# Kernel optimization log

Hardware: AMD Instinct MI355X
Metric: run time of the kernel (lower is better)

Reference implementation:

```python
import jax, jax.numpy as jnp
import numpy as np

N_NODES = 100000
N_EDGES = 100000
N_MAP = 128
EPS = 1e-5


def _gn1(x, g, b):
    # GroupNorm with 1 group == per-row normalization over channels, affine per channel
    m = jnp.mean(x, axis=-1, keepdims=True)
    v = jnp.mean((x - m) ** 2, axis=-1, keepdims=True)
    return (x - m) * jax.lax.rsqrt(v + EPS) * g + b


def setup_inputs() -> dict:
    key = jax.random.key(0)
    ks = jax.random.split(key, 16)
    s = 0.02
    d = N_MAP
    inp = {
        'nodes': jax.random.normal(ks[0], (N_NODES, 8), jnp.float32),
        'indexes': jax.random.randint(ks[1], (N_EDGES, 28), 0, N_NODES, jnp.int64)
            if jax.config.jax_enable_x64 else jax.random.randint(ks[1], (N_EDGES, 28), 0, N_NODES, jnp.int32),
        'mask': jnp.full((14,), N_EDGES, dtype=jnp.int32),
        'in1_W': jax.random.normal(ks[2], (d, 2), jnp.float32) * s,
        'in1_b': jnp.zeros((d,), jnp.float32),
        'in2_W': jax.random.normal(ks[3], (d, d), jnp.float32) * s,
        'in_g': jnp.ones((d,), jnp.float32),
        'in_bg': jnp.zeros((d,), jnp.float32),
        'seg1_W': jax.random.normal(ks[4], (d, 2), jnp.float32) * s,
        'seg1_b': jnp.zeros((d,), jnp.float32),
        'seg2_W': jax.random.normal(ks[5], (d, d), jnp.float32) * s,
        'seg_g': jnp.ones((d,), jnp.float32),
        'seg_bg': jnp.zeros((d,), jnp.float32),
        'meta_W': jax.random.normal(ks[6], (d, d + 4), jnp.float32) * s,
        'meta_g': jnp.ones((d,), jnp.float32),
        'meta_bg': jnp.zeros((d,), jnp.float32),
        'ctr_W': jax.random.normal(ks[7], (4, d, d), jnp.float32) * s,
        'edge_W': jax.random.normal(ks[8], (4, 14, d, d), jnp.float32) * s,
        'norm_g': jnp.ones((4, d), jnp.float32),
        'norm_bg': jnp.zeros((4, d), jnp.float32),
        'ctr2_W': jax.random.normal(ks[9], (4, d, d), jnp.float32) * s,
        'ctr2_g': jnp.ones((4, d), jnp.float32),
        'ctr2_bg': jnp.zeros((4, d), jnp.float32),
    }
    return inp


def reference(nodes, indexes, mask, in1_W, in1_b, in2_W, in_g, in_bg,
              seg1_W, seg1_b, seg2_W, seg_g, seg_bg, meta_W, meta_g, meta_bg,
              ctr_W, edge_W, norm_g, norm_bg, ctr2_W, ctr2_g, ctr2_bg):
    relu = jax.nn.relu
    # input / seg branches: Linear+ReLU then bias-free Linear + GroupNorm(1)
    feat = _gn1(relu(nodes[:, :2] @ in1_W.T + in1_b) @ in2_W.T, in_g, in_bg)
    feat = feat + _gn1(relu(nodes[:, 2:4] @ seg1_W.T + seg1_b) @ seg2_W.T, seg_g, seg_bg)
    feat = relu(feat)
    # meta: Linear(n_map+4 -> n_map, bias-free) + GN + ReLU
    feat = relu(_gn1(jnp.concatenate([feat, nodes[:, 4:]], axis=1) @ meta_W.T, meta_g, meta_bg))
    res = feat
    E = indexes.shape[0]
    eid = jnp.arange(E)
    for i in range(4):
        temp = feat @ ctr_W[i].T
        # 14 edge types in column order: pre0..pre5, right, suc0..suc5, left
        for t in range(14):
            valid = (eid < mask[t])[:, None]          # [E,1]
            src = jnp.where(valid[:, 0], indexes[:, 2 * t + 1], 0)
            dst = jnp.where(valid[:, 0], indexes[:, 2 * t], 0)
            msg = jnp.where(valid, feat[src] @ edge_W[i, t].T, 0.0)  # [E, d]
            temp = temp.at[dst].add(msg)
        feat = relu(_gn1(temp, norm_g[i], norm_bg[i]))
        feat = _gn1(feat @ ctr2_W[i].T, ctr2_g[i], ctr2_bg[i])
        feat = relu(feat + res)
        res = feat
    return (feat, nodes[:, :2])
```

## Files before the change

kernel.cpp:

```cpp
#include <hip/hip_runtime.h>
#include <hip/hip_bf16.h>

#define NN 100000
#define NE 100000
#define NCNT (14 * NN)
#define LP 136
#define LP2 168
#define SCAN_CHUNK 4096
#define NSCB ((NCNT + SCAN_CHUNK - 1) / SCAN_CHUNK)

typedef __bf16 bf16;
typedef __bf16 bf16x8 __attribute__((ext_vector_type(8)));
typedef float  f32x4  __attribute__((ext_vector_type(4)));


template<int PITCH, int COLS>
__device__ inline void stageWB(const bf16* __restrict__ Wg, bf16* Wl) {
    constexpr int NV = 128 * COLS / 8;
    for (int i = threadIdx.x; i < NV; i += 256) {
        const int e = i * 8;
        const int r = e / COLS, c = e % COLS;
        *(float4*)(&Wl[r * PITCH + c]) = ((const float4*)Wg)[i];
    }
}

__device__ inline void stageA(const bf16* __restrict__ A, bf16* Al, int row0) {
    const int r = threadIdx.x >> 2, q = threadIdx.x & 3;
    float4* d = (float4*)(&Al[r * LP + q * 32]);
    const int row = row0 + r;
    if (row < NN) {
        const float4* s = (const float4*)(A + (size_t)row * 128 + q * 32);
        float4 a0 = s[0], a1 = s[1], a2 = s[2], a3 = s[3];
        d[0] = a0; d[1] = a1; d[2] = a2; d[3] = a3;
    } else {
        float4 z = {0.f, 0.f, 0.f, 0.f};
        d[0] = z; d[1] = z; d[2] = z; d[3] = z;
    }
}

template<int PITCH, int KSTEPS>
__device__ inline void mmaT(const bf16* Al, const bf16* Wl, int m0, int lane, f32x4 acc[8]) {
#pragma unroll
    for (int kk = 0; kk < KSTEPS; ++kk) {
        bf16x8 a = *(const bf16x8*)(&Al[(m0 + (lane & 15)) * PITCH + kk * 32 + (lane >> 4) * 8]);
#pragma unroll
        for (int n = 0; n < 8; ++n) {
            bf16x8 b = *(const bf16x8*)(&Wl[(n * 16 + (lane & 15)) * PITCH + kk * 32 + (lane >> 4) * 8]);
            acc[n] = __builtin_amdgcn_mfma_f32_16x16x32_bf16(a, b, acc[n], 0, 0, 0);
        }
    }
}

__device__ inline void zacc(f32x4 acc[8]) {
    f32x4 z = {0.f, 0.f, 0.f, 0.f};
#pragma unroll
    for (int n = 0; n < 8; ++n) acc[n] = z;
}

__device__ inline void gnstats(const f32x4 acc[8], float mean[4], float rs[4]) {
    float s1[4], s2[4];
#pragma unroll
    for (int r = 0; r < 4; ++r) { s1[r] = 0.f; s2[r] = 0.f; }
#pragma unroll
    for (int n = 0; n < 8; ++n)
#pragma unroll
        for (int r = 0; r < 4; ++r) { float v = acc[n][r]; s1[r] += v; s2[r] += v * v; }
#pragma unroll
    for (int off = 1; off < 16; off <<= 1) {
#pragma unroll
        for (int r = 0; r < 4; ++r) {
            s1[r] += __shfl_xor(s1[r], off, 64);
            s2[r] += __shfl_xor(s2[r], off, 64);
        }
    }
#pragma unroll
    for (int r = 0; r < 4; ++r) {
        const float m = s1[r] * 0.0078125f;
        const float v = fmaxf(s2[r] * 0.0078125f - m * m, 0.f);
        mean[r] = m;
        rs[r] = rsqrtf(v + 1e-5f);
    }
}


__global__ void k_cvt(const float* __restrict__ s, bf16* __restrict__ d, int n) {
    for (int i = blockIdx.x * 256 + threadIdx.x; i < n; i += gridDim.x * 256)
        d[i] = (bf16)s[i];
}

__global__ void k_cvt_meta(const float* __restrict__ s, bf16* __restrict__ d) {
    for (int i = blockIdx.x * 256 + threadIdx.x; i < 128 * 160; i += gridDim.x * 256) {
        const int r = i / 160, c = i % 160;
        d[i] = (bf16)(c < 132 ? s[r * 132 + c] : 0.f);
    }
}


__global__ __launch_bounds__(256) void k_count(const int* __restrict__ idx,
                                               const int* __restrict__ mask,
                                               int* __restrict__ cnt) {
    __shared__ int lim[14];
    if (threadIdx.x < 14) lim[threadIdx.x] = min(mask[threadIdx.x], NE);
    __syncthreads();
    for (int i = blockIdx.x * 256 + threadIdx.x; i < 14 * NE; i += gridDim.x * 256) {
        const int e = i / 14, t = i - e * 14;
        if (e < lim[t]) atomicAdd(&cnt[t * NN + idx[(size_t)e * 28 + 2 * t]], 1);
    }
}

__global__ __launch_bounds__(256) void k_scanA(const int* __restrict__ cnt,
                                               int* __restrict__ ptr,
                                               int* __restrict__ tot) {
    __shared__ int sm[256];
    const int tid = threadIdx.x;
    const int base = blockIdx.x * SCAN_CHUNK + tid * 16;
    int v[16]; int run = 0;
#pragma unroll
    for (int j = 0; j < 16; ++j) {
        const int x = (base + j < NCNT) ? cnt[base + j] : 0;
        v[j] = run; run += x;
    }
    sm[tid] = run; __syncthreads();
    for (int d = 1; d < 256; d <<= 1) {
        int t = 0;
        if (tid >= d) t = sm[tid - d];
        __syncthreads();
        sm[tid] += t;
        __syncthreads();
    }
    const int off = sm[tid] - run;
#pragma unroll
    for (int j = 0; j < 16; ++j)
        if (base + j < NCNT) ptr[base + j] = v[j] + off;
    if (tid == 255) tot[blockIdx.x] = sm[255];
}

__global__ void k_scanB(int* __restrict__ tot) {
    if (threadIdx.x == 0 && blockIdx.x == 0) {
        int acc = 0;
        for (int b = 0; b < NSCB; ++b) { const int t = tot[b]; tot[b] = acc; acc += t; }
        tot[NSCB] = acc;
    }
}

__global__ __launch_bounds__(256) void k_scanC(int* __restrict__ ptr,
                                               int* __restrict__ cursor,
                                               const int* __restrict__ tot) {
    const int base = blockIdx.x * SCAN_CHUNK;
    const int o = tot[blockIdx.x];
    for (int j = threadIdx.x; j < SCAN_CHUNK; j += 256) {
        const int i = base + j;
        if (i < NCNT) { const int p = ptr[i] + o; ptr[i] = p; cursor[i] = p; }
    }
    if (blockIdx.x == 0 && threadIdx.x == 0) ptr[NCNT] = tot[NSCB];
}

__global__ __launch_bounds__(256) void k_fill(const int* __restrict__ idx,
                                              const int* __restrict__ mask,
                                              int* __restrict__ cursor,
                                              int* __restrict__ elist) {
    __shared__ int lim[14];
    if (threadIdx.x < 14) lim[threadIdx.x] = min(mask[threadIdx.x], NE);
    __syncthreads();
    for (int i = blockIdx.x * 256 + threadIdx.x; i < 14 * NE; i += gridDim.x * 256) {
        const int e = i / 14, t = i - e * 14;
        if (e < lim[t]) {
            const int dst = idx[(size_t)e * 28 + 2 * t];
            const int pos = atomicAdd(&cursor[t * NN + dst], 1);
            elist[pos] = e;
        }
    }
}

__global__ __launch_bounds__(256) void k_sortseg(const int* __restrict__ ptr,
                                                 int* __restrict__ elist,
                                                 const int* __restrict__ idx) {
    for (int i = blockIdx.x * 256 + threadIdx.x; i < NCNT; i += gridDim.x * 256) {
        const int s = ptr[i], e2 = ptr[i + 1];
        for (int a = s + 1; a < e2; ++a) {
            const int key = elist[a];
            int b = a - 1;
            while (b >= s && elist[b] > key) { elist[b + 1] = elist[b]; --b; }
            elist[b + 1] = key;
        }
        const int t = i / NN;
        for (int j = s; j < e2; ++j)
            elist[j] = idx[(size_t)elist[j] * 28 + 2 * t + 1];
    }
}


__global__ __launch_bounds__(256) void k_in(
    const float* __restrict__ nodes,
    const float* __restrict__ in1W, const float* __restrict__ in1b,
    const bf16* __restrict__ wIn2,
    const float* __restrict__ ing, const float* __restrict__ inbg,
    const float* __restrict__ seg1W, const float* __restrict__ seg1b,
    const bf16* __restrict__ wSeg2,
    const float* __restrict__ segg, const float* __restrict__ segbg,
    bf16* __restrict__ outPre)
{
    __shared__ __align__(16) bf16 Wl[128 * LP];
    __shared__ __align__(16) bf16 Al[64 * LP];
    __shared__ float w0[128], w1[128], bb[128];
    __shared__ float xs[64][4];
    const int tid = threadIdx.x;
    const int row0 = blockIdx.x * 64;
    if (tid < 64) {
        const int row = row0 + tid;
        float4 x = {0.f, 0.f, 0.f, 0.f};
        if (row < NN) x = *(const float4*)(nodes + (size_t)row * 8);
        xs[tid][0] = x.x; xs[tid][1] = x.y; xs[tid][2] = x.z; xs[tid][3] = x.w;
    }
    if (tid < 128) { w0[tid] = in1W[tid * 2]; w1[tid] = in1W[tid * 2 + 1]; bb[tid] = in1b[tid]; }
    stageWB<LP, 128>(wIn2, Wl);
    __syncthreads();
    for (int i = tid; i < 64 * 128; i += 256) {
        const int r = i >> 7, j = i & 127;
        Al[r * LP + j] = (bf16)fmaxf(xs[r][0] * w0[j] + xs[r][1] * w1[j] + bb[j], 0.f);
    }
    __syncthreads();
    const int lane = tid & 63, m0 = (tid >> 6) * 16;
    f32x4 accP[8]; zacc(accP);
    mmaT<LP, 4>(Al, Wl, m0, lane, accP);
    __syncthreads();
    if (tid < 128) { w0[tid] = seg1W[tid * 2]; w1[tid] = seg1W[tid * 2 + 1]; bb[tid] = seg1b[tid]; }
    stageWB<LP, 128>(wSeg2, Wl);
    __syncthreads();
    for (int i = tid; i < 64 * 128; i += 256) {
        const int r = i >> 7, j = i & 127;
        Al[r * LP + j] = (bf16)fmaxf(xs[r][2] * w0[j] + xs[r][3] * w1[j] + bb[j], 0.f);
    }
    __syncthreads();
    f32x4 accQ[8]; zacc(accQ);
    mmaT<LP, 4>(Al, Wl, m0, lane, accQ);

    float mP[4], rP[4], mQ[4], rQ[4];
    gnstats(accP, mP, rP);
    gnstats(accQ, mQ, rQ);
    float gP[8], bP[8], gQ[8], bQ[8];
#pragma unroll
    for (int n = 0; n < 8; ++n) {
        const int c = n * 16 + (lane & 15);
        gP[n] = ing[c]; bP[n] = inbg[c]; gQ[n] = segg[c]; bQ[n] = segbg[c];
    }
#pragma unroll
    for (int r = 0; r < 4; ++r) {
        const int row = row0 + m0 + (lane >> 4) * 4 + r;
        if (row < NN) {
#pragma unroll
            for (int n = 0; n < 8; ++n) {
                const float yp = (accP[n][r] - mP[r]) * rP[r] * gP[n] + bP[n];
                const float yq = (accQ[n][r] - mQ[r]) * rQ[r] * gQ[n] + bQ[n];
                outPre[(size_t)row * 128 + n * 16 + (lane & 15)] = (bf16)fmaxf(yp + yq, 0.f);
            }
        }
    }
}


__global__ __launch_bounds__(256) void k_meta(
    const bf16* __restrict__ Apre, const float* __restrict__ nodes,
    const bf16* __restrict__ Wg,
    const float* __restrict__ g, const float* __restrict__ bg,
    float* __restrict__ featF, bf16* __restrict__ featB)
{
    __shared__ __align__(16) bf16 Wl[128 * LP2];
    __shared__ __align__(16) bf16 Al[64 * LP2];
    const int row0 = blockIdx.x * 64;
    stageWB<LP2, 160>(Wg, Wl);
    {
        const int r = threadIdx.x >> 2, q = threadIdx.x & 3;
        float4* d = (float4*)(&Al[r * LP2 + q * 32]);
        const int row = row0 + r;
        if (row < NN) {
            const float4* s = (const float4*)(Apre + (size_t)row * 128 + q * 32);
            float4 a0 = s[0], a1 = s[1], a2 = s[2], a3 = s[3];
            d[0] = a0; d[1] = a1; d[2] = a2; d[3] = a3;
        } else {
            float4 z = {0.f, 0.f, 0.f, 0.f};
            d[0] = z; d[1] = z; d[2] = z; d[3] = z;
        }
    }
    if (threadIdx.x < 64) {
        const int rr = threadIdx.x, row = row0 + rr;
        bf16* d = &Al[rr * LP2 + 128];
        if (row < NN) {
            const float4 x = *(const float4*)(nodes + (size_t)row * 8 + 4);
            d[0] = (bf16)x.x; d[1] = (bf16)x.y; d[2] = (bf16)x.z; d[3] = (bf16)x.w;
        } else {
            d[0] = (bf16)0.f; d[1] = (bf16)0.f; d[2] = (bf16)0.f; d[3] = (bf16)0.f;
        }
#pragma unroll
        for (int c = 4; c < 32; ++c) d[c] = (bf16)0.f;
    }
    __syncthreads();
    const int lane = threadIdx.x & 63, m0 = (threadIdx.x >> 6) * 16;
    f32x4 acc[8]; zacc(acc);
    mmaT<LP2, 5>(Al, Wl, m0, lane, acc);

    float mean[4], rs[4];
    gnstats(acc, mean, rs);
    float gv[8], bv[8];
#pragma unroll
    for (int n = 0; n < 8; ++n) { const int c = n * 16 + (lane & 15); gv[n] = g[c]; bv[n] = bg[c]; }
#pragma unroll
    for (int r = 0; r < 4; ++r) {
        const int row = row0 + m0 + (lane >> 4) * 4 + r;
        if (row < NN) {
            const size_t off = (size_t)row * 128 + (lane & 15);
#pragma unroll
            for (int n = 0; n < 8; ++n) {
                const float y = (acc[n][r] - mean[r]) * rs[r] * gv[n] + bv[n];
                const float o = fmaxf(y, 0.f);
                featF[off + n * 16] = o;
                featB[off + n * 16] = (bf16)o;
            }
        }
    }
}


__global__ __launch_bounds__(256) void k_round(
    const bf16* __restrict__ feat,
    const int* __restrict__ ptr,
    const int* __restrict__ slist,
    const bf16* __restrict__ wEdgeR,
    const bf16* __restrict__ wCtrR,
    const bf16* __restrict__ wCtr2R,
    const float* __restrict__ ng, const float* __restrict__ nbg,
    const float* __restrict__ c2g, const float* __restrict__ c2bg,
    float* __restrict__ featF,
    bf16* __restrict__ featOut)
{
    __shared__ __align__(16) bf16 Wl[128 * LP];
    __shared__ __align__(16) bf16 Al[64 * LP];
    const int tid = threadIdx.x, lane = tid & 63, m0 = (tid >> 6) * 16;
    const int row0 = blockIdx.x * 64;
    const int rr = tid >> 2, q = tid & 3;
    const int dst = row0 + rr;

    f32x4 acc[8]; zacc(acc);

    for (int t = 0; t < 14; ++t) {
        __syncthreads();
        stageWB<LP, 128>(wEdgeR + (size_t)t * 16384, Wl);
        float ag[32];
#pragma unroll
        for (int j = 0; j < 32; ++j) ag[j] = 0.f;
        if (dst < NN) {
            const int p0 = ptr[t * NN + dst], p1 = ptr[t * NN + dst + 1];
            for (int j = p0; j < p1; ++j) {
                const bf16x8* fp = (const bf16x8*)(feat + (size_t)slist[j] * 128 + q * 32);
                bf16x8 a0 = fp[0], a1 = fp[1], a2 = fp[2], a3 = fp[3];
#pragma unroll
                for (int k2 = 0; k2 < 8; ++k2) {
                    ag[k2]      += (float)a0[k2];
                    ag[8 + k2]  += (float)a1[k2];
                    ag[16 + k2] += (float)a2[k2];
                    ag[24 + k2] += (float)a3[k2];
                }
            }
        }
        bf16x8 ov[4];
#pragma unroll
        for (int v = 0; v < 4; ++v)
#pragma unroll
            for (int k2 = 0; k2 < 8; ++k2) ov[v][k2] = (bf16)ag[v * 8 + k2];
        bf16x8* dp = (bf16x8*)(&Al[rr * LP + q * 32]);
        dp[0] = ov[0]; dp[1] = ov[1]; dp[2] = ov[2]; dp[3] = ov[3];
        __syncthreads();
        mmaT<LP, 4>(Al, Wl, m0, lane, acc);
    }
    __syncthreads();
    stageWB<LP, 128>(wCtrR, Wl);
    stageA(feat, Al, row0);
    __syncthreads();
    mmaT<LP, 4>(Al, Wl, m0, lane, acc);

    float mean[4], rs[4];
    gnstats(acc, mean, rs);
    float gv[8], bv[8];
#pragma unroll
    for (int n = 0; n < 8; ++n) { const int c = n * 16 + (lane & 15); gv[n] = ng[c]; bv[n] = nbg[c]; }
    __syncthreads();
#pragma unroll
    for (int r = 0; r < 4; ++r) {
        const int lrow = m0 + (lane >> 4) * 4 + r;
#pragma unroll
        for (int n = 0; n < 8; ++n) {
            const float y = (acc[n][r] - mean[r]) * rs[r] * gv[n] + bv[n];
            Al[lrow * LP + n * 16 + (lane & 15)] = (bf16)fmaxf(y, 0.f);
        }
    }
    stageWB<LP, 128>(wCtr2R, Wl);
    __syncthreads();

    zacc(acc);
    mmaT<LP, 4>(Al, Wl, m0, lane, acc);

    gnstats(acc, mean, rs);
#pragma unroll
    for (int n = 0; n < 8; ++n) { const int c = n * 16 + (lane & 15); gv[n] = c2g[c]; bv[n] = c2bg[c]; }
#pragma unroll
    for (int r = 0; r < 4; ++r) {
        const int row = row0 + m0 + (lane >> 4) * 4 + r;
        if (row < NN) {
            const size_t off = (size_t)row * 128 + (lane & 15);
#pragma unroll
            for (int n = 0; n < 8; ++n) {
                const float y = (acc[n][r] - mean[r]) * rs[r] * gv[n] + bv[n];
                const float o = fmaxf(y + featF[off + n * 16], 0.f);
                featF[off + n * 16] = o;
                featOut[off + n * 16] = (bf16)o;
            }
        }
    }
}


__global__ void k_out(const float* __restrict__ featF, const float* __restrict__ nodes,
                      float* __restrict__ out)
{
    const size_t stride = (size_t)gridDim.x * 256;
    size_t tid = (size_t)blockIdx.x * 256 + threadIdx.x;
    for (size_t i = tid; i < 12800000 / 4; i += stride)
        ((float4*)out)[i] = ((const float4*)featF)[i];
    for (size_t j = tid; j < 200000; j += stride)
        out[12800000 + j] = nodes[(j >> 1) * 8 + (j & 1)];
}


extern "C" void kernel_launch(void* const* d_in, const int* in_sizes, int n_in,
                              void* d_out, int out_size, void* d_ws, size_t ws_size,
                              hipStream_t stream) {
    const float* nodes  = (const float*)d_in[0];
    const int*   idx    = (const int*)d_in[1];
    const int*   mask   = (const int*)d_in[2];
    const float* in1W   = (const float*)d_in[3];
    const float* in1b   = (const float*)d_in[4];
    const float* in2W   = (const float*)d_in[5];
    const float* ing    = (const float*)d_in[6];
    const float* inbg   = (const float*)d_in[7];
    const float* seg1W  = (const float*)d_in[8];
    const float* seg1b  = (const float*)d_in[9];
    const float* seg2W  = (const float*)d_in[10];
    const float* segg   = (const float*)d_in[11];
    const float* segbg  = (const float*)d_in[12];
    const float* metaW  = (const float*)d_in[13];
    const float* metag  = (const float*)d_in[14];
    const float* metabg = (const float*)d_in[15];
    const float* ctrW   = (const float*)d_in[16];
    const float* edgeW  = (const float*)d_in[17];
    const float* normg  = (const float*)d_in[18];
    const float* normbg = (const float*)d_in[19];
    const float* ctr2W  = (const float*)d_in[20];
    const float* ctr2g  = (const float*)d_in[21];
    const float* ctr2bg = (const float*)d_in[22];
    float* out = (float*)d_out;

    char* w = (char*)d_ws;
    float* featF  = (float*)w; w += (size_t)NN * 128 * 4;
    bf16*  featB0 = (bf16*)w;  w += (size_t)NN * 128 * 2;
    bf16*  featB1 = (bf16*)w;  w += (size_t)NN * 128 * 2;
    bf16*  preB   = (bf16*)w;  w += (size_t)NN * 128 * 2;
    bf16*  wIn2   = (bf16*)w;  w += 16384 * 2;
    bf16*  wSeg2  = (bf16*)w;  w += 16384 * 2;
    bf16*  wMeta  = (bf16*)w;  w += 20480 * 2;
    bf16*  wCtr   = (bf16*)w;  w += 65536 * 2;
    bf16*  wCtr2  = (bf16*)w;  w += 65536 * 2;
    bf16*  wEdge  = (bf16*)w;  w += (size_t)917504 * 2;
    int*   cnt    = (int*)w;   w += (size_t)NCNT * 4;
    int*   ptr    = (int*)w;   w += ((size_t)NCNT + 4) * 4;
    int*   cursor = (int*)w;   w += (size_t)NCNT * 4;
    int*   elist  = (int*)w;   w += (size_t)14 * NE * 4;
    int*   tot    = (int*)w;   w += (NSCB + 1) * 4;

    dim3 blk(256);
    const int gRows = (NN + 63) / 64;

    hipMemsetAsync(cnt, 0, (size_t)NCNT * 4, stream);
    k_count<<<2048, blk, 0, stream>>>(idx, mask, cnt);
    k_scanA<<<NSCB, blk, 0, stream>>>(cnt, ptr, tot);
    k_scanB<<<1, 64, 0, stream>>>(tot);
    k_scanC<<<NSCB, blk, 0, stream>>>(ptr, cursor, tot);
    k_fill<<<2048, blk, 0, stream>>>(idx, mask, cursor, elist);
    k_sortseg<<<2048, blk, 0, stream>>>(ptr, elist, idx);

    k_cvt<<<64, blk, 0, stream>>>(in2W, wIn2, 16384);
    k_cvt<<<64, blk, 0, stream>>>(seg2W, wSeg2, 16384);
    k_cvt_meta<<<80, blk, 0, stream>>>(metaW, wMeta);
    k_cvt<<<256, blk, 0, stream>>>(ctrW, wCtr, 65536);
    k_cvt<<<256, blk, 0, stream>>>(ctr2W, wCtr2, 65536);
    k_cvt<<<2048, blk, 0, stream>>>(edgeW, wEdge, 917504);

    k_in<<<gRows, blk, 0, stream>>>(nodes, in1W, in1b, wIn2, ing, inbg,
                                    seg1W, seg1b, wSeg2, segg, segbg, preB);
    k_meta<<<gRows, blk, 0, stream>>>(preB, nodes, wMeta, metag, metabg, featF, featB0);

    bf16* bufs[2] = { featB0, featB1 };
    for (int i = 0; i < 4; ++i) {
        k_round<<<gRows, blk, 0, stream>>>(bufs[i & 1], ptr, elist,
                                           wEdge + (size_t)i * 14 * 16384,
                                           wCtr + (size_t)i * 16384,
                                           wCtr2 + (size_t)i * 16384,
                                           normg + i * 128, normbg + i * 128,
                                           ctr2g + i * 128, ctr2bg + i * 128,
                                           featF, bufs[(i + 1) & 1]);
    }
    k_out<<<4096, blk, 0, stream>>>(featF, nodes, out);
}
```

Measured before the change: 1.272 ms.

## Restructure message-passing round with async double-buffered LDS weights and register-resident aggregation

Rewrites the per-round kernel to use 512-thread blocks over 128 rows, staging each edge-type weight matrix into XOR-swizzled LDS with global_load_lds, double-buffered so the next type's weights load while the current MFMA runs. Gathered neighbour sums now stay in registers as MFMA A fragments instead of passing through LDS, and the centre-node term is folded in as a fifteenth pass. The last round writes the fp32 output directly, so the separate copy kernel is replaced by a small kernel that only copies node coordinates. This trades higher register and LDS pressure and more complex barrier handling for less LDS traffic and fewer synchronisations.

```diff
diff --git a/kernel.cpp b/kernel.cpp
--- a/kernel.cpp
+++ b/kernel.cpp
@@ -14,6 +14,44 @@
 typedef float  f32x4  __attribute__((ext_vector_type(4)));
 
 
+__device__ __forceinline__ void gl2lds16(const bf16* g, bf16* l) {
+    __builtin_amdgcn_global_load_lds(
+        (const __attribute__((address_space(1))) void*)g,
+        (__attribute__((address_space(3))) void*)l, 16, 0, 0);
+}
+
+__device__ __forceinline__ void zacc8(f32x4 acc[8]) {
+    f32x4 z = {0.f, 0.f, 0.f, 0.f};
+#pragma unroll
+    for (int n = 0; n < 8; ++n) acc[n] = z;
+}
+
+__device__ __forceinline__ void gnstats(const f32x4 acc[8], float mean[4], float rs[4]) {
+    float s1[4], s2[4];
+#pragma unroll
+    for (int r = 0; r < 4; ++r) { s1[r] = 0.f; s2[r] = 0.f; }
+#pragma unroll
+    for (int n = 0; n < 8; ++n)
+#pragma unroll
+        for (int r = 0; r < 4; ++r) { float v = acc[n][r]; s1[r] += v; s2[r] += v * v; }
+#pragma unroll
+    for (int off = 1; off < 16; off <<= 1) {
+#pragma unroll
+        for (int r = 0; r < 4; ++r) {
+            s1[r] += __shfl_xor(s1[r], off, 64);
+            s2[r] += __shfl_xor(s2[r], off, 64);
+        }
+    }
+#pragma unroll
+    for (int r = 0; r < 4; ++r) {
+        const float m = s1[r] * 0.0078125f;
+        const float v = fmaxf(s2[r] * 0.0078125f - m * m, 0.f);
+        mean[r] = m;
+        rs[r] = rsqrtf(v + 1e-5f);
+    }
+}
+
+
 template<int PITCH, int COLS>
 __device__ inline void stageWB(const bf16* __restrict__ Wg, bf16* Wl) {
     constexpr int NV = 128 * COLS / 8;
@@ -24,20 +62,6 @@
     }
 }
 
-__device__ inline void stageA(const bf16* __restrict__ A, bf16* Al, int row0) {
-    const int r = threadIdx.x >> 2, q = threadIdx.x & 3;
-    float4* d = (float4*)(&Al[r * LP + q * 32]);
-    const int row = row0 + r;
-    if (row < NN) {
-        const float4* s = (const float4*)(A + (size_t)row * 128 + q * 32);
-        float4 a0 = s[0], a1 = s[1], a2 = s[2], a3 = s[3];
-        d[0] = a0; d[1] = a1; d[2] = a2; d[3] = a3;
-    } else {
-        float4 z = {0.f, 0.f, 0.f, 0.f};
-        d[0] = z; d[1] = z; d[2] = z; d[3] = z;
-    }
-}
-
 template<int PITCH, int KSTEPS>
 __device__ inline void mmaT(const bf16* Al, const bf16* Wl, int m0, int lane, f32x4 acc[8]) {
 #pragma unroll
@@ -51,34 +75,39 @@
     }
 }
 
-__device__ inline void zacc(f32x4 acc[8]) {
-    f32x4 z = {0.f, 0.f, 0.f, 0.f};
-#pragma unroll
-    for (int n = 0; n < 8; ++n) acc[n] = z;
-}
-
-__device__ inline void gnstats(const f32x4 acc[8], float mean[4], float rs[4]) {
-    float s1[4], s2[4];
-#pragma unroll
-    for (int r = 0; r < 4; ++r) { s1[r] = 0.f; s2[r] = 0.f; }
-#pragma unroll
-    for (int n = 0; n < 8; ++n)
-#pragma unroll
-        for (int r = 0; r < 4; ++r) { float v = acc[n][r]; s1[r] += v; s2[r] += v * v; }
-#pragma unroll
-    for (int off = 1; off < 16; off <<= 1) {
-#pragma unroll
-        for (int r = 0; r < 4; ++r) {
-            s1[r] += __shfl_xor(s1[r], off, 64);
-            s2[r] += __shfl_xor(s2[r], off, 64);
-        }
-    }
-#pragma unroll
-    for (int r = 0; r < 4; ++r) {
-        const float m = s1[r] * 0.0078125f;
-        const float v = fmaxf(s2[r] * 0.0078125f - m * m, 0.f);
-        mean[r] = m;
-        rs[r] = rsqrtf(v + 1e-5f);
+
+__device__ __forceinline__ void stageW(const bf16* __restrict__ Wg, bf16* WLbase,
+                                       int w, int lane) {
+#pragma unroll
+    for (int k = 0; k < 4; ++k) {
+        const int R = (w * 4 + k) * 4 + (lane >> 4);
+        const int sg = (lane & 15) ^ ((k & 1) * 4 + (lane >> 4));
+        gl2lds16(Wg + R * 128 + sg * 8, WLbase + (w * 4 + k) * 512);
+    }
+}
+
+__device__ __forceinline__ void mmaW(const bf16* B, const bf16x8 afr[4],
+                                     int r, int h, int r7, f32x4 acc[8]) {
+#pragma unroll
+    for (int kk = 0; kk < 4; ++kk) {
+        const int sl = ((kk * 4 + h) ^ r7) * 8;
+#pragma unroll
+        for (int n = 0; n < 8; ++n) {
+            const bf16x8 b = *(const bf16x8*)(B + (n * 16 + r) * 128 + sl);
+            acc[n] = __builtin_amdgcn_mfma_f32_16x16x32_bf16(afr[kk], b, acc[n], 0, 0, 0);
+        }
+    }
+}
+
+__device__ __forceinline__ void accum_row(const bf16* __restrict__ rp, float ag[4][8]) {
+    const bf16x8* q = (const bf16x8*)rp;
+    bf16x8 v0 = q[0], v1 = q[4], v2 = q[8], v3 = q[12];
+#pragma unroll
+    for (int e = 0; e < 8; ++e) {
+        ag[0][e] += (float)v0[e];
+        ag[1][e] += (float)v1[e];
+        ag[2][e] += (float)v2[e];
+        ag[3][e] += (float)v3[e];
     }
 }
 
@@ -221,7 +250,7 @@
     }
     __syncthreads();
     const int lane = tid & 63, m0 = (tid >> 6) * 16;
-    f32x4 accP[8]; zacc(accP);
+    f32x4 accP[8]; zacc8(accP);
     mmaT<LP, 4>(Al, Wl, m0, lane, accP);
     __syncthreads();
     if (tid < 128) { w0[tid] = seg1W[tid * 2]; w1[tid] = seg1W[tid * 2 + 1]; bb[tid] = seg1b[tid]; }
@@ -232,7 +261,7 @@
         Al[r * LP + j] = (bf16)fmaxf(xs[r][2] * w0[j] + xs[r][3] * w1[j] + bb[j], 0.f);
     }
     __syncthreads();
-    f32x4 accQ[8]; zacc(accQ);
+    f32x4 accQ[8]; zacc8(accQ);
     mmaT<LP, 4>(Al, Wl, m0, lane, accQ);
 
     float mP[4], rP[4], mQ[4], rQ[4];
@@ -296,7 +325,7 @@
     }
     __syncthreads();
     const int lane = threadIdx.x & 63, m0 = (threadIdx.x >> 6) * 16;
-    f32x4 acc[8]; zacc(acc);
+    f32x4 acc[8]; zacc8(acc);
     mmaT<LP2, 5>(Al, Wl, m0, lane, acc);
 
     float mean[4], rs[4];
@@ -321,7 +350,7 @@
 }
 
 
-__global__ __launch_bounds__(256) void k_round(
+__global__ __launch_bounds__(512, 4) void k_round(
     const bf16* __restrict__ feat,
     const int* __restrict__ ptr,
     const int* __restrict__ slist,
@@ -331,103 +360,132 @@
     const float* __restrict__ ng, const float* __restrict__ nbg,
     const float* __restrict__ c2g, const float* __restrict__ c2bg,
     float* __restrict__ featF,
-    bf16* __restrict__ featOut)
+    bf16* __restrict__ featOut,
+    float* __restrict__ outF,
+    int last)
 {
-    __shared__ __align__(16) bf16 Wl[128 * LP];
-    __shared__ __align__(16) bf16 Al[64 * LP];
-    const int tid = threadIdx.x, lane = tid & 63, m0 = (tid >> 6) * 16;
-    const int row0 = blockIdx.x * 64;
-    const int rr = tid >> 2, q = tid & 3;
-    const int dst = row0 + rr;
-
-    f32x4 acc[8]; zacc(acc);
-
-    for (int t = 0; t < 14; ++t) {
-        __syncthreads();
-        stageWB<LP, 128>(wEdgeR + (size_t)t * 16384, Wl);
-        float ag[32];
-#pragma unroll
-        for (int j = 0; j < 32; ++j) ag[j] = 0.f;
-        if (dst < NN) {
-            const int p0 = ptr[t * NN + dst], p1 = ptr[t * NN + dst + 1];
-            for (int j = p0; j < p1; ++j) {
-                const bf16x8* fp = (const bf16x8*)(feat + (size_t)slist[j] * 128 + q * 32);
-                bf16x8 a0 = fp[0], a1 = fp[1], a2 = fp[2], a3 = fp[3];
-#pragma unroll
-                for (int k2 = 0; k2 < 8; ++k2) {
-                    ag[k2]      += (float)a0[k2];
-                    ag[8 + k2]  += (float)a1[k2];
-                    ag[16 + k2] += (float)a2[k2];
-                    ag[24 + k2] += (float)a3[k2];
+    __shared__ __align__(16) bf16 WL[2 * 16384];
+    const int tid = threadIdx.x;
+    const int w = tid >> 6, lane = tid & 63;
+    const int r = lane & 15, h = lane >> 4, r7 = r & 7;
+    const int m0 = w * 16;
+    const int row0 = blockIdx.x * 128;
+    const int grow = row0 + m0 + r;
+    const bool rowok = grow < NN;
+
+    stageW(wEdgeR, WL, w, lane);
+
+    int p0 = 0, p1 = 0;
+    if (rowok) { p0 = ptr[grow]; p1 = ptr[grow + 1]; }
+    int sA = slist[p1 > p0 ? p0 : 0];
+
+    f32x4 acc[8]; zacc8(acc);
+
+    for (int t = 0; t < 15; ++t) {
+        float ag[4][8];
+#pragma unroll
+        for (int kk = 0; kk < 4; ++kk)
+#pragma unroll
+            for (int e = 0; e < 8; ++e) ag[kk][e] = 0.f;
+
+        if (t < 14) {
+            if (rowok && p1 > p0) {
+                accum_row(feat + (size_t)sA * 128 + h * 8, ag);
+                for (int j = p0 + 1; j < p1; ++j)
+                    accum_row(feat + (size_t)slist[j] * 128 + h * 8, ag);
+            }
+        } else if (rowok) {
+            accum_row(feat + (size_t)grow * 128 + h * 8, ag);
+        }
+
+        if (t < 13) {
+            int q0 = 0, q1 = 0;
+            if (rowok) {
+                const size_t i2 = (size_t)(t + 1) * NN + grow;
+                q0 = ptr[i2]; q1 = ptr[i2 + 1];
+            }
+            const int sN = slist[q1 > q0 ? q0 : 0];
+            p0 = q0; p1 = q1; sA = sN;
+        }
+
+        bf16x8 afr[4];
+#pragma unroll
+        for (int kk = 0; kk < 4; ++kk)
+#pragma unroll
+            for (int e = 0; e < 8; ++e) afr[kk][e] = (bf16)ag[kk][e];
+
+        asm volatile("s_waitcnt vmcnt(0)" ::: "memory");
+        __builtin_amdgcn_s_barrier();
+        __builtin_amdgcn_sched_barrier(0);
+        if (t < 13)       stageW(wEdgeR + (size_t)(t + 1) * 16384, WL + ((t + 1) & 1) * 16384, w, lane);
+        else if (t == 13) stageW(wCtrR,  WL,          w, lane);
+        else              stageW(wCtr2R, WL + 16384,  w, lane);
+        __builtin_amdgcn_sched_barrier(0);
+        mmaW(WL + (t & 1) * 16384, afr, r, h, r7, acc);
+    }
+
+    float mean[4], rsv[4];
+    gnstats(acc, mean, rsv);
+    float gv[8], bv[8];
+#pragma unroll
+    for (int n = 0; n < 8; ++n) { const int c = n * 16 + r; gv[n] = ng[c]; bv[n] = nbg[c]; }
+    asm volatile("s_waitcnt vmcnt(0)" ::: "memory");
+    __builtin_amdgcn_s_barrier();
+    __builtin_amdgcn_sched_barrier(0);
+#pragma unroll
+    for (int r2 = 0; r2 < 4; ++r2) {
+        const int lrow = m0 + h * 4 + r2;
+#pragma unroll
+        for (int n = 0; n < 8; ++n) {
+            const float y = (acc[n][r2] - mean[r2]) * rsv[r2] * gv[n] + bv[n];
+            const int col = n * 16 + r;
+            const int slot = (col >> 3) ^ (lrow & 7);
+            *(bf16*)((char*)WL + lrow * 256 + slot * 16 + (col & 7) * 2) = (bf16)fmaxf(y, 0.f);
+        }
+    }
+    asm volatile("s_waitcnt lgkmcnt(0)" ::: "memory");
+    __builtin_amdgcn_s_barrier();
+    __builtin_amdgcn_sched_barrier(0);
+
+    bf16x8 afr2[4];
+    {
+        const int arow = m0 + r;
+#pragma unroll
+        for (int kk = 0; kk < 4; ++kk) {
+            const int slot = (kk * 4 + h) ^ (arow & 7);
+            afr2[kk] = *(const bf16x8*)((const char*)WL + arow * 256 + slot * 16);
+        }
+    }
+    zacc8(acc);
+    mmaW(WL + 16384, afr2, r, h, r7, acc);
+
+    gnstats(acc, mean, rsv);
+#pragma unroll
+    for (int n = 0; n < 8; ++n) { const int c = n * 16 + r; gv[n] = c2g[c]; bv[n] = c2bg[c]; }
+#pragma unroll
+    for (int r2 = 0; r2 < 4; ++r2) {
+        const int orow = row0 + m0 + h * 4 + r2;
+        if (orow < NN) {
+            const size_t off = (size_t)orow * 128 + r;
+#pragma unroll
+            for (int n = 0; n < 8; ++n) {
+                const float y = (acc[n][r2] - mean[r2]) * rsv[r2] * gv[n] + bv[n];
+                const float o = fmaxf(y + featF[off + n * 16], 0.f);
+                if (last) {
+                    outF[off + n * 16] = o;
+                } else {
+                    featF[off + n * 16] = o;
+                    featOut[off + n * 16] = (bf16)o;
                 }
             }
         }
-        bf16x8 ov[4];
-#pragma unroll
-        for (int v = 0; v < 4; ++v)
-#pragma unroll
-            for (int k2 = 0; k2 < 8; ++k2) ov[v][k2] = (bf16)ag[v * 8 + k2];
-        bf16x8* dp = (bf16x8*)(&Al[rr * LP + q * 32]);
-        dp[0] = ov[0]; dp[1] = ov[1]; dp[2] = ov[2]; dp[3] = ov[3];
-        __syncthreads();
-        mmaT<LP, 4>(Al, Wl, m0, lane, acc);
-    }
-    __syncthreads();
-    stageWB<LP, 128>(wCtrR, Wl);
-    stageA(feat, Al, row0);
-    __syncthreads();
-    mmaT<LP, 4>(Al, Wl, m0, lane, acc);
-
-    float mean[4], rs[4];
-    gnstats(acc, mean, rs);
-    float gv[8], bv[8];
-#pragma unroll
-    for (int n = 0; n < 8; ++n) { const int c = n * 16 + (lane & 15); gv[n] = ng[c]; bv[n] = nbg[c]; }
-    __syncthreads();
-#pragma unroll
-    for (int r = 0; r < 4; ++r) {
-        const int lrow = m0 + (lane >> 4) * 4 + r;
-#pragma unroll
-        for (int n = 0; n < 8; ++n) {
-            const float y = (acc[n][r] - mean[r]) * rs[r] * gv[n] + bv[n];
-            Al[lrow * LP + n * 16 + (lane & 15)] = (bf16)fmaxf(y, 0.f);
-        }
-    }
-    stageWB<LP, 128>(wCtr2R, Wl);
-    __syncthreads();
-
-    zacc(acc);
-    mmaT<LP, 4>(Al, Wl, m0, lane, acc);
-
-    gnstats(acc, mean, rs);
-#pragma unroll
-    for (int n = 0; n < 8; ++n) { const int c = n * 16 + (lane & 15); gv[n] = c2g[c]; bv[n] = c2bg[c]; }
-#pragma unroll
-    for (int r = 0; r < 4; ++r) {
-        const int row = row0 + m0 + (lane >> 4) * 4 + r;
-        if (row < NN) {
-            const size_t off = (size_t)row * 128 + (lane & 15);
-#pragma unroll
-            for (int n = 0; n < 8; ++n) {
-                const float y = (acc[n][r] - mean[r]) * rs[r] * gv[n] + bv[n];
-                const float o = fmaxf(y + featF[off + n * 16], 0.f);
-                featF[off + n * 16] = o;
-                featOut[off + n * 16] = (bf16)o;
-            }
-        }
-    }
-}
-
-
-__global__ void k_out(const float* __restrict__ featF, const float* __restrict__ nodes,
-                      float* __restrict__ out)
-{
-    const size_t stride = (size_t)gridDim.x * 256;
-    size_t tid = (size_t)blockIdx.x * 256 + threadIdx.x;
-    for (size_t i = tid; i < 12800000 / 4; i += stride)
-        ((float4*)out)[i] = ((const float4*)featF)[i];
-    for (size_t j = tid; j < 200000; j += stride)
-        out[12800000 + j] = nodes[(j >> 1) * 8 + (j & 1)];
+    }
+}
+
+
+__global__ void k_nodes(const float* __restrict__ nodes, float* __restrict__ out) {
+    const int j = blockIdx.x * 256 + threadIdx.x;
+    if (j < 2 * NN) out[(size_t)NN * 128 + j] = nodes[(size_t)(j >> 1) * 8 + (j & 1)];
 }
 
 
@@ -499,14 +557,16 @@
     k_meta<<<gRows, blk, 0, stream>>>(preB, nodes, wMeta, metag, metabg, featF, featB0);
 
     bf16* bufs[2] = { featB0, featB1 };
+    const int gR2 = (NN + 127) / 128;
     for (int i = 0; i < 4; ++i) {
-        k_round<<<gRows, blk, 0, stream>>>(bufs[i & 1], ptr, elist,
-                                           wEdge + (size_t)i * 14 * 16384,
-                                           wCtr + (size_t)i * 16384,
-                                           wCtr2 + (size_t)i * 16384,
-                                           normg + i * 128, normbg + i * 128,
-                                           ctr2g + i * 128, ctr2bg + i * 128,
-                                           featF, bufs[(i + 1) & 1]);
-    }
-    k_out<<<4096, blk, 0, stream>>>(featF, nodes, out);
-}
+        k_round<<<gR2, dim3(512), 0, stream>>>(bufs[i & 1], ptr, elist,
+                                               wEdge + (size_t)i * 14 * 16384,
+                                               wCtr + (size_t)i * 16384,
+                                               wCtr2 + (size_t)i * 16384,
+                                               normg + i * 128, normbg + i * 128,
+                                               ctr2g + i * 128, ctr2bg + i * 128,
+                                               featF, bufs[(i + 1) & 1], out,
+                                               i == 3 ? 1 : 0);
+    }
+    k_nodes<<<(2 * NN + 255) / 256, blk, 0, stream>>>(nodes, out);
+}
```

Result: faster. 1.074 ms (-15.6%).
